# Optimization experiments

Hardware: AMD Instinct MI355X
Metric: run time of the kernel (lower is better)

The kernel has to match this reference:

```python
import jax, jax.numpy as jnp
import numpy as np

N_NODES = 100000
N_EDGES = 1600000
IN_CH = 128
HID = 128
OUT_CH = 64
N_GRAPHS = 512


def gcn_conv(x, edge_index, W, b):
    # GCNConv (PyG defaults): add self-loops, symmetric normalization
    # out = D^{-1/2} (A + I) D^{-1/2} X W + b
    n = x.shape[0]
    loop = jnp.arange(n, dtype=edge_index.dtype)
    src = jnp.concatenate([edge_index[0], loop])
    dst = jnp.concatenate([edge_index[1], loop])
    deg = jax.ops.segment_sum(jnp.ones_like(dst, x.dtype), dst, num_segments=n)
    dinv = jnp.where(deg > 0, jax.lax.rsqrt(deg), jnp.zeros_like(deg))
    norm = dinv[src] * dinv[dst]            # [E+N]
    h = x @ W                                # [N, out] transform first (dense GEMM)
    msg = h[src] * norm[:, None]             # gather + scale  [E+N, out]
    return jax.ops.segment_sum(msg, dst, num_segments=n) + b


def global_mean_pool(x, batch, num_graphs):
    sums = jax.ops.segment_sum(x, batch, num_segments=num_graphs)
    cnts = jax.ops.segment_sum(jnp.ones_like(batch, x.dtype), batch, num_segments=num_graphs)
    return sums / jnp.maximum(cnts, 1.0)[:, None]


def setup_inputs() -> dict:
    key = jax.random.key(0)
    ks = jax.random.split(key, 12)
    x = jax.random.normal(ks[0], (N_NODES, IN_CH), dtype=jnp.float32)
    edge_index = jax.random.randint(ks[1], (2, N_EDGES), 0, N_NODES, dtype=jnp.int64)
    batch = jnp.sort(jax.random.randint(ks[2], (N_NODES,), 0, N_GRAPHS, dtype=jnp.int64))
    def glorot(k, fi, fo):
        s = float(np.sqrt(6.0 / (fi + fo)))
        return jax.random.uniform(k, (fi, fo), jnp.float32, -s, s)
    W1 = glorot(ks[3], IN_CH, HID); b1 = jnp.zeros((HID,), jnp.float32)
    W2 = glorot(ks[4], HID, HID);   b2 = jnp.zeros((HID,), jnp.float32)
    W3 = glorot(ks[5], HID, HID);   b3 = jnp.zeros((HID,), jnp.float32)
    W4 = glorot(ks[6], HID, OUT_CH); b4 = jnp.zeros((OUT_CH,), jnp.float32)
    return {"x": x, "edge_index": edge_index, "batch": batch,
            "W1": W1, "b1": b1, "W2": W2, "b2": b2,
            "W3": W3, "b3": b3, "W4": W4, "b4": b4}


def reference(x, edge_index, batch, W1, b1, W2, b2, W3, b3, W4, b4):
    h = jax.nn.relu(gcn_conv(x, edge_index, W1, b1))
    h = jax.nn.relu(gcn_conv(h, edge_index, W2, b2))
    g = global_mean_pool(h, batch, N_GRAPHS)           # [G, HID]
    # MLP head; Dropout(0.2) is identity in eval mode
    g = jax.nn.relu(g @ W3 + b3)
    return g @ W4 + b4                                  # [G, OUT_CH]
```

## Files before the change

### kernel.cpp

```cpp
#include <hip/hip_runtime.h>

#define NN 100000
#define EE 1600000
#define CH 128
#define NG 512
#define OC 64

#define CSH 10
#define NCB 98
#define PBLK 256
#define PCHUNK 6250
#define SCAP 128

#define O_DINV   0
#define O_ROWS   100032
#define O_CNT    200064
#define O_PART   225152
#define O_OFFS   225280
#define O_START  225408
#define O_CSR    225984
#define O_HS     2726016
#define O_STG    9126080
#define O_WT1    9126080
#define O_WT2    9142464
#define O_A1     14800448

typedef __attribute__((ext_vector_type(8))) short short8v;
typedef __attribute__((ext_vector_type(4))) float float4v;

static __device__ __forceinline__ unsigned short f2bf(float x) {
  unsigned u = __float_as_uint(x);
  return (unsigned short)((u + 0x7FFFu + ((u >> 16) & 1u)) >> 16);
}
static __device__ __forceinline__ float bf2f(unsigned short h) {
  return __uint_as_float((unsigned)h << 16);
}
static __device__ __forceinline__ unsigned pack2(float a, float b) {
  return (unsigned)f2bf(a) | ((unsigned)f2bf(b) << 16);
}
static __device__ __forceinline__ float bflo(unsigned v) {
  return __uint_as_float(v << 16);
}
static __device__ __forceinline__ float bfhi(unsigned v) {
  return __uint_as_float(v & 0xFFFF0000u);
}

__global__ __launch_bounds__(1024) void k_part(const int* __restrict__ src,
                                               const int* __restrict__ dst,
                                               int* __restrict__ cnt,
                                               unsigned* __restrict__ stg) {
  __shared__ int hist[NCB];
  __shared__ int lcur[NCB];
  __shared__ unsigned lout[PCHUNK];
  int t = threadIdx.x;
  int e0 = blockIdx.x * PCHUNK;
  if (t < NCB) { hist[t] = 0; lcur[t] = 0; }
  __syncthreads();
  for (int e = e0 + t; e < e0 + PCHUNK; e += 1024)
    atomicAdd(&hist[dst[e] >> CSH], 1);
  __syncthreads();
  if (t == 0) {
    int s = 0;
    for (int i = 0; i < NCB; ++i) { int v = hist[i]; hist[i] = s; s += v; }
  }
  __syncthreads();
  for (int e = e0 + t; e < e0 + PCHUNK; e += 1024) {
    int d = dst[e];
    int b = d >> CSH;
    int p = hist[b] + atomicAdd(&lcur[b], 1);
    lout[p] = (unsigned)src[e] | ((unsigned)(d & 1023) << 17);
  }
  __syncthreads();
  int w = t >> 6, lane = t & 63;
  unsigned* mystg = stg + (size_t)blockIdx.x * NCB * SCAP;
  for (int b = w; b < NCB; b += 16) {
    int beg = hist[b];
    int end = (b == NCB - 1) ? PCHUNK : hist[b + 1];
    int n = min(end - beg, SCAP);
    for (int i = lane; i < n; i += 64) mystg[b * SCAP + i] = lout[beg + i];
    if (lane == 0) cnt[blockIdx.x * NCB + b] = n;
  }
}

__global__ __launch_bounds__(1024) void k_count(const unsigned* __restrict__ stg,
                                                const int* __restrict__ cnt,
                                                int* __restrict__ rows,
                                                int* __restrict__ part,
                                                float* __restrict__ dinv) {
  __shared__ int ldeg[1024];
  __shared__ int s[1024];
  int b = blockIdx.x;
  int t = threadIdx.x;
  int w = t >> 6, lane = t & 63;
  int gid = (b << CSH) + t;
  ldeg[t] = 0;
  __syncthreads();
  for (int blk = w; blk < PBLK; blk += 16) {
    int c = cnt[blk * NCB + b];
    const unsigned* p = stg + ((size_t)blk * NCB + b) * SCAP;
    for (int e = lane; e < c; e += 64) atomicAdd(&ldeg[p[e] >> 17], 1);
  }
  __syncthreads();
  int v = ldeg[t];
  if (gid < NN) dinv[gid] = rsqrtf((float)(v + 1));
  int pdeg = (v + 7) & ~7;
  s[t] = pdeg;
  __syncthreads();
  for (int off = 1; off < 1024; off <<= 1) {
    int u = (t >= off) ? s[t - off] : 0;
    __syncthreads();
    if (t >= off) s[t] += u;
    __syncthreads();
  }
  if (gid < NN) rows[gid] = s[t] - pdeg;
  if (t == 1023) part[b] = s[t];
}

__global__ void k_scan_part(const int* __restrict__ part, int* __restrict__ offs) {
  __shared__ int s[128];
  int t = threadIdx.x;
  int v = (t < NCB) ? part[t] : 0;
  s[t] = v;
  __syncthreads();
  for (int off = 1; off < 128; off <<= 1) {
    int u = (t >= off) ? s[t - off] : 0;
    __syncthreads();
    if (t >= off) s[t] += u;
    __syncthreads();
  }
  if (t < NCB) offs[t] = s[t] - v;
}

__global__ void k_scan_add(int* __restrict__ rows, const int* __restrict__ offs,
                           const int* __restrict__ part,
                           const int* __restrict__ batch, int* __restrict__ start) {
  int i = blockIdx.x * 256 + threadIdx.x;
  if (i >= NN) return;
  rows[i] += offs[i >> 10];
  if (i == 0) rows[NN] = offs[NCB - 1] + part[NCB - 1];
  int b = batch[i];
  int prev = (i == 0) ? -1 : batch[i - 1];
  for (int g = prev + 1; g <= b; ++g) start[g] = i;
  if (i == NN - 1)
    for (int g = b + 1; g <= NG; ++g) start[g] = NN;
}

__global__ __launch_bounds__(1024) void k_place(const unsigned* __restrict__ stg,
                                                const int* __restrict__ cnt,
                                                const int* __restrict__ rows,
                                                int* __restrict__ csr) {
  __shared__ int lrow[1024];
  __shared__ int lcur[1024];
  int b = blockIdx.x;
  int t = threadIdx.x;
  int w = t >> 6, lane = t & 63;
  int gid = (b << CSH) + t;
  lrow[t] = (gid < NN) ? rows[gid] : 0;
  lcur[t] = 0;
  __syncthreads();
  for (int blk = w; blk < PBLK; blk += 16) {
    int c = cnt[blk * NCB + b];
    const unsigned* p = stg + ((size_t)blk * NCB + b) * SCAP;
    for (int e = lane; e < c; e += 64) {
      unsigned x = p[e];
      int ld = x >> 17;
      int q = atomicAdd(&lcur[ld], 1);
      csr[lrow[ld] + q] = (int)(x & 0x1FFFFu);
    }
  }
  __syncthreads();
  int d = lcur[t];
  int pd = (d + 7) & ~7;
  int base = lrow[t];
  for (int i = d; i < pd; ++i) csr[base + i] = NN;
}

__global__ void k_wsplit(const float* __restrict__ W1, const float* __restrict__ W2,
                         unsigned short* __restrict__ wt1,
                         unsigned short* __restrict__ wt2) {
  int id = blockIdx.x * 256 + threadIdx.x;
  const float* W = (id < 16384) ? W1 : W2;
  unsigned short* wt = (id < 16384) ? wt1 : wt2;
  int i = id & 16383;
  int k = i >> 7, n = i & 127;
  float w = W[i];
  unsigned short h = f2bf(w);
  unsigned short l = f2bf(w - bf2f(h));
  wt[n * 128 + k] = h;
  wt[16384 + n * 128 + k] = l;
}

__global__ __launch_bounds__(256) void k_gemm_mfma(
    const float* __restrict__ X, const unsigned short* __restrict__ wth,
    const unsigned short* __restrict__ wtl, const float* __restrict__ dinv,
    unsigned short* __restrict__ Hs) {
  __shared__ __align__(16) unsigned short sWh[64 * 136];
  __shared__ __align__(16) unsigned short sWl[64 * 136];
  __shared__ __align__(16) unsigned short sXh[128 * 40];
  __shared__ __align__(16) unsigned short sXl[128 * 40];

  const int t = threadIdx.x;
  const int w = t >> 6, lane = t & 63;
  const int quad = lane >> 4, lr = lane & 15;
  const int row0 = blockIdx.x * 128;
  const int col0 = blockIdx.y * 64;

  if (blockIdx.x == 0 && blockIdx.y == 0 && t < 64)
    *(unsigned*)&Hs[(size_t)NN * CH + t * 2] = 0u;

#pragma unroll
  for (int j = 0; j < 8; ++j) {
    int id = t + j * 256;
    int n = id >> 5, kk = (id & 31) * 4;
    *(ushort4*)&sWh[n * 136 + kk] = *(const ushort4*)&wth[(col0 + n) * 128 + kk];
    *(ushort4*)&sWl[n * 136 + kk] = *(const ushort4*)&wtl[(col0 + n) * 128 + kk];
  }

  float4v acc[2][4];
#pragma unroll
  for (int mi = 0; mi < 2; ++mi)
#pragma unroll
    for (int ni = 0; ni < 4; ++ni) acc[mi][ni] = (float4v){0.f, 0.f, 0.f, 0.f};

  for (int ks = 0; ks < 4; ++ks) {
    const int k0 = ks * 32;
    if (ks) __syncthreads();
#pragma unroll
    for (int i = 0; i < 4; ++i) {
      int row = i * 32 + (t >> 3);
      int seg = t & 7;
      int gr = row0 + row;
      float4 xv = {0.f, 0.f, 0.f, 0.f};
      if (gr < NN) xv = *(const float4*)&X[(size_t)gr * CH + k0 + seg * 4];
      ushort4 h, l;
      h.x = f2bf(xv.x); l.x = f2bf(xv.x - bf2f(h.x));
      h.y = f2bf(xv.y); l.y = f2bf(xv.y - bf2f(h.y));
      h.z = f2bf(xv.z); l.z = f2bf(xv.z - bf2f(h.z));
      h.w = f2bf(xv.w); l.w = f2bf(xv.w - bf2f(h.w));
      *(ushort4*)&sXh[row * 40 + seg * 4] = h;
      *(ushort4*)&sXl[row * 40 + seg * 4] = l;
    }
    __syncthreads();

    short8v ah[2], al[2];
#pragma unroll
    for (int mi = 0; mi < 2; ++mi) {
      int r = w * 32 + mi * 16 + lr;
      ah[mi] = *(const short8v*)&sXh[r * 40 + quad * 8];
      al[mi] = *(const short8v*)&sXl[r * 40 + quad * 8];
    }
#pragma unroll
    for (int ni = 0; ni < 4; ++ni) {
      int n = ni * 16 + lr;
      short8v bh = *(const short8v*)&sWh[n * 136 + k0 + quad * 8];
      short8v bl = *(const short8v*)&sWl[n * 136 + k0 + quad * 8];
#pragma unroll
      for (int mi = 0; mi < 2; ++mi) {
        acc[mi][ni] = __builtin_amdgcn_mfma_f32_16x16x32_bf16(ah[mi], bh, acc[mi][ni], 0, 0, 0);
        acc[mi][ni] = __builtin_amdgcn_mfma_f32_16x16x32_bf16(ah[mi], bl, acc[mi][ni], 0, 0, 0);
        acc[mi][ni] = __builtin_amdgcn_mfma_f32_16x16x32_bf16(al[mi], bh, acc[mi][ni], 0, 0, 0);
      }
    }
  }

#pragma unroll
  for (int mi = 0; mi < 2; ++mi) {
#pragma unroll
    for (int r = 0; r < 4; ++r) {
      int grow = row0 + w * 32 + mi * 16 + quad * 4 + r;
      if (grow < NN) {
        float d = dinv[grow];
#pragma unroll
        for (int ni = 0; ni < 4; ++ni)
          Hs[(size_t)grow * CH + col0 + ni * 16 + lr] = f2bf(d * acc[mi][ni][r]);
      }
    }
  }
}

__global__ __launch_bounds__(256) void k_gemm_bf(
    const unsigned short* __restrict__ A, const unsigned short* __restrict__ wth,
    const unsigned short* __restrict__ wtl, const float* __restrict__ dinv,
    unsigned short* __restrict__ Hs) {
  __shared__ __align__(16) unsigned short sWh[64 * 136];
  __shared__ __align__(16) unsigned short sWl[64 * 136];
  __shared__ __align__(16) unsigned short sA[128 * 40];

  const int t = threadIdx.x;
  const int w = t >> 6, lane = t & 63;
  const int quad = lane >> 4, lr = lane & 15;
  const int row0 = blockIdx.x * 128;
  const int col0 = blockIdx.y * 64;

  if (blockIdx.x == 0 && blockIdx.y == 0 && t < 64)
    *(unsigned*)&Hs[(size_t)NN * CH + t * 2] = 0u;

#pragma unroll
  for (int j = 0; j < 8; ++j) {
    int id = t + j * 256;
    int n = id >> 5, kk = (id & 31) * 4;
    *(ushort4*)&sWh[n * 136 + kk] = *(const ushort4*)&wth[(col0 + n) * 128 + kk];
    *(ushort4*)&sWl[n * 136 + kk] = *(const ushort4*)&wtl[(col0 + n) * 128 + kk];
  }

  float4v acc[2][4];
#pragma unroll
  for (int mi = 0; mi < 2; ++mi)
#pragma unroll
    for (int ni = 0; ni < 4; ++ni) acc[mi][ni] = (float4v){0.f, 0.f, 0.f, 0.f};

  for (int ks = 0; ks < 4; ++ks) {
    const int k0 = ks * 32;
    if (ks) __syncthreads();
#pragma unroll
    for (int i = 0; i < 2; ++i) {
      int id = t + i * 256;
      int row = id >> 2, seg = id & 3;
      int gr = row0 + row;
      ushort4 v = {0, 0, 0, 0};
      if (gr < NN) v = *(const ushort4*)&A[(size_t)gr * CH + k0 + seg * 8];
      *(ushort4*)&sA[row * 40 + seg * 8] = v;
      ushort4 v2 = {0, 0, 0, 0};
      if (gr < NN) v2 = *(const ushort4*)&A[(size_t)gr * CH + k0 + seg * 8 + 4];
      *(ushort4*)&sA[row * 40 + seg * 8 + 4] = v2;
    }
    __syncthreads();

    short8v ah[2];
#pragma unroll
    for (int mi = 0; mi < 2; ++mi) {
      int r = w * 32 + mi * 16 + lr;
      ah[mi] = *(const short8v*)&sA[r * 40 + quad * 8];
    }
#pragma unroll
    for (int ni = 0; ni < 4; ++ni) {
      int n = ni * 16 + lr;
      short8v bh = *(const short8v*)&sWh[n * 136 + k0 + quad * 8];
      short8v bl = *(const short8v*)&sWl[n * 136 + k0 + quad * 8];
#pragma unroll
      for (int mi = 0; mi < 2; ++mi) {
        acc[mi][ni] = __builtin_amdgcn_mfma_f32_16x16x32_bf16(ah[mi], bh, acc[mi][ni], 0, 0, 0);
        acc[mi][ni] = __builtin_amdgcn_mfma_f32_16x16x32_bf16(ah[mi], bl, acc[mi][ni], 0, 0, 0);
      }
    }
  }

#pragma unroll
  for (int mi = 0; mi < 2; ++mi) {
#pragma unroll
    for (int r = 0; r < 4; ++r) {
      int grow = row0 + w * 32 + mi * 16 + quad * 4 + r;
      if (grow < NN) {
        float d = dinv[grow];
#pragma unroll
        for (int ni = 0; ni < 4; ++ni)
          Hs[(size_t)grow * CH + col0 + ni * 16 + lr] = f2bf(d * acc[mi][ni][r]);
      }
    }
  }
}

__global__ __launch_bounds__(256) void k_aggregate(
    const uint2* __restrict__ H2, const int* __restrict__ rows,
    const int* __restrict__ csr, const float* __restrict__ dinv,
    const float* __restrict__ bias, uint2* __restrict__ out) {
  int node = blockIdx.x * 4 + (threadIdx.x >> 6);
  if (node >= NN) return;
  int lane = threadIdx.x & 63;
  int h = lane >> 5, li = lane & 31;
  float a0 = 0.f, a1 = 0.f, a2 = 0.f, a3 = 0.f;
  int e0 = rows[node], e1 = rows[node + 1];
  int nr = (e1 - e0) >> 3;
  if (nr) {
    const int* cp = csr + e0 + h;
    uint2 va[4], vb[4];

#define LOADQ(buf)                                                          \
  do {                                                                      \
    unsigned s0_ = (unsigned)cp[0], s1_ = (unsigned)cp[2];                  \
    unsigned s2_ = (unsigned)cp[4], s3_ = (unsigned)cp[6];                  \
    buf[0] = H2[(s0_ << 5) | li];                                           \
    buf[1] = H2[(s1_ << 5) | li];                                           \
    buf[2] = H2[(s2_ << 5) | li];                                           \
    buf[3] = H2[(s3_ << 5) | li];                                           \
    cp += 8;                                                                \
  } while (0)

#define ACCQ(buf)                                                           \
  do {                                                                      \
    _Pragma("unroll")                                                       \
    for (int k_ = 0; k_ < 4; ++k_) {                                        \
      a0 += bflo(buf[k_].x); a1 += bfhi(buf[k_].x);                         \
      a2 += bflo(buf[k_].y); a3 += bfhi(buf[k_].y);                         \
    }                                                                       \
  } while (0)

    LOADQ(va);
    int rem = nr - 1;
    while (rem >= 2) {
      LOADQ(vb); ACCQ(va);
      LOADQ(va); ACCQ(vb);
      rem -= 2;
    }
    if (rem) { LOADQ(vb); ACCQ(va); ACCQ(vb); }
    else     { ACCQ(va); }
#undef LOADQ
#undef ACCQ
  }
  a0 += __shfl_xor(a0, 32);
  a1 += __shfl_xor(a1, 32);
  a2 += __shfl_xor(a2, 32);
  a3 += __shfl_xor(a3, 32);
  uint2 sv = H2[((unsigned)node << 5) | li];
  a0 += bflo(sv.x); a1 += bfhi(sv.x);
  a2 += bflo(sv.y); a3 += bfhi(sv.y);
  float d = dinv[node];
  float4 b4 = *(const float4*)&bias[li << 2];
  float o0 = fmaxf(fmaf(d, a0, b4.x), 0.f);
  float o1 = fmaxf(fmaf(d, a1, b4.y), 0.f);
  float o2 = fmaxf(fmaf(d, a2, b4.z), 0.f);
  float o3 = fmaxf(fmaf(d, a3, b4.w), 0.f);
  if (!h)
    out[((unsigned)node << 5) | li] = make_uint2(pack2(o0, o1), pack2(o2, o3));
}

__global__ __launch_bounds__(256) void k_head(
    const unsigned short* __restrict__ A, const int* __restrict__ start,
    const float* __restrict__ W3, const float* __restrict__ b3,
    const float* __restrict__ W4, const float* __restrict__ b4,
    float* __restrict__ out) {
  __shared__ float pooled[128];
  __shared__ float part[128];
  __shared__ float g1[128];
  int g = blockIdx.x;
  int c = threadIdx.x & 127;
  int half = threadIdx.x >> 7;
  int s0 = start[g], s1 = start[g + 1];
  float sum = 0.f;
  for (int i = s0 + half; i < s1; i += 2)
    sum += bf2f(A[(size_t)i * CH + c]);
  if (half) part[c] = sum;
  __syncthreads();
  if (!half) {
    float n = fmaxf((float)(s1 - s0), 1.0f);
    pooled[c] = (sum + part[c]) / n;
  }
  __syncthreads();
  if (threadIdx.x < 128) {
    float acc = b3[c];
    for (int k = 0; k < 128; ++k) acc += pooled[k] * W3[k * CH + c];
    g1[c] = fmaxf(acc, 0.f);
  }
  __syncthreads();
  if (threadIdx.x < 64) {
    float acc = b4[threadIdx.x];
    for (int k = 0; k < 128; ++k) acc += g1[k] * W4[k * OC + threadIdx.x];
    out[(size_t)g * OC + threadIdx.x] = acc;
  }
}

extern "C" void kernel_launch(void* const* d_in, const int* in_sizes, int n_in,
                              void* d_out, int out_size, void* d_ws, size_t ws_size,
                              hipStream_t stream) {
  const float* X   = (const float*)d_in[0];
  const int* ei    = (const int*)d_in[1];
  const int* batch = (const int*)d_in[2];
  const float* W1  = (const float*)d_in[3];
  const float* b1  = (const float*)d_in[4];
  const float* W2  = (const float*)d_in[5];
  const float* b2  = (const float*)d_in[6];
  const float* W3  = (const float*)d_in[7];
  const float* b3  = (const float*)d_in[8];
  const float* W4  = (const float*)d_in[9];
  const float* b4  = (const float*)d_in[10];
  float* out = (float*)d_out;
  float* ws = (float*)d_ws;

  const int* src = ei;
  const int* dst = ei + EE;

  float* dinv = ws + O_DINV;
  int* rows   = (int*)(ws + O_ROWS);
  int* cnt    = (int*)(ws + O_CNT);
  int* part   = (int*)(ws + O_PART);
  int* offs   = (int*)(ws + O_OFFS);
  int* start  = (int*)(ws + O_START);
  int* csr    = (int*)(ws + O_CSR);
  unsigned short* Hs = (unsigned short*)(ws + O_HS);
  unsigned* stg = (unsigned*)(ws + O_STG);
  unsigned short* wt1 = (unsigned short*)(ws + O_WT1);
  unsigned short* wt2 = (unsigned short*)(ws + O_WT2);
  unsigned short* A1 = (unsigned short*)(ws + O_A1);

  k_part<<<PBLK, 1024, 0, stream>>>(src, dst, cnt, stg);
  k_count<<<NCB, 1024, 0, stream>>>(stg, cnt, rows, part, dinv);
  k_scan_part<<<1, 128, 0, stream>>>(part, offs);
  k_scan_add<<<(NN + 255) / 256, 256, 0, stream>>>(rows, offs, part, batch, start);
  k_place<<<NCB, 1024, 0, stream>>>(stg, cnt, rows, csr);
  k_wsplit<<<128, 256, 0, stream>>>(W1, W2, wt1, wt2);

  dim3 ggrid((NN + 127) / 128, 2);
  k_gemm_mfma<<<ggrid, 256, 0, stream>>>(X, wt1, wt1 + 16384, dinv, Hs);
  k_aggregate<<<(NN + 3) / 4, 256, 0, stream>>>((const uint2*)Hs, rows, csr, dinv, b1, (uint2*)A1);
  k_gemm_bf<<<ggrid, 256, 0, stream>>>(A1, wt2, wt2 + 16384, dinv, Hs);
  k_aggregate<<<(NN + 3) / 4, 256, 0, stream>>>((const uint2*)Hs, rows, csr, dinv, b2, (uint2*)A1);

  k_head<<<NG, 256, 0, stream>>>(A1, start, W3, b3, W4, b4, out);
}
```

Before: 376.8 us.

## Compute full 128-column GEMM tiles per block with weights read from global memory; vectorize pooling

The two GEMM kernels now compute all 128 output columns per block instead of splitting columns across two blocks. This halves the grid and removes the redundant X load and bf16 split per column half. Weight fragments are read directly from global memory (through cache) instead of being staged in shared memory, which drops the weight LDS fill but doubles the accumulator registers and may lower occupancy. The head kernel's mean pooling now uses 16 row-groups with 8-wide vector loads and a shared-memory reduction, in place of two scalar-load halves.

```diff
diff --git a/kernel.cpp b/kernel.cpp
--- a/kernel.cpp
+++ b/kernel.cpp
@@ -194,8 +194,6 @@
     const float* __restrict__ X, const unsigned short* __restrict__ wth,
     const unsigned short* __restrict__ wtl, const float* __restrict__ dinv,
     unsigned short* __restrict__ Hs) {
-  __shared__ __align__(16) unsigned short sWh[64 * 136];
-  __shared__ __align__(16) unsigned short sWl[64 * 136];
   __shared__ __align__(16) unsigned short sXh[128 * 40];
   __shared__ __align__(16) unsigned short sXl[128 * 40];
 
@@ -203,24 +201,15 @@
   const int w = t >> 6, lane = t & 63;
   const int quad = lane >> 4, lr = lane & 15;
   const int row0 = blockIdx.x * 128;
-  const int col0 = blockIdx.y * 64;
-
-  if (blockIdx.x == 0 && blockIdx.y == 0 && t < 64)
+
+  if (blockIdx.x == 0 && t < 64)
     *(unsigned*)&Hs[(size_t)NN * CH + t * 2] = 0u;
 
-#pragma unroll
-  for (int j = 0; j < 8; ++j) {
-    int id = t + j * 256;
-    int n = id >> 5, kk = (id & 31) * 4;
-    *(ushort4*)&sWh[n * 136 + kk] = *(const ushort4*)&wth[(col0 + n) * 128 + kk];
-    *(ushort4*)&sWl[n * 136 + kk] = *(const ushort4*)&wtl[(col0 + n) * 128 + kk];
-  }
-
-  float4v acc[2][4];
+  float4v acc[2][8];
 #pragma unroll
   for (int mi = 0; mi < 2; ++mi)
 #pragma unroll
-    for (int ni = 0; ni < 4; ++ni) acc[mi][ni] = (float4v){0.f, 0.f, 0.f, 0.f};
+    for (int ni = 0; ni < 8; ++ni) acc[mi][ni] = (float4v){0.f, 0.f, 0.f, 0.f};
 
   for (int ks = 0; ks < 4; ++ks) {
     const int k0 = ks * 32;
@@ -250,10 +239,10 @@
       al[mi] = *(const short8v*)&sXl[r * 40 + quad * 8];
     }
 #pragma unroll
-    for (int ni = 0; ni < 4; ++ni) {
+    for (int ni = 0; ni < 8; ++ni) {
       int n = ni * 16 + lr;
-      short8v bh = *(const short8v*)&sWh[n * 136 + k0 + quad * 8];
-      short8v bl = *(const short8v*)&sWl[n * 136 + k0 + quad * 8];
+      short8v bh = *(const short8v*)&wth[n * 128 + k0 + quad * 8];
+      short8v bl = *(const short8v*)&wtl[n * 128 + k0 + quad * 8];
 #pragma unroll
       for (int mi = 0; mi < 2; ++mi) {
         acc[mi][ni] = __builtin_amdgcn_mfma_f32_16x16x32_bf16(ah[mi], bh, acc[mi][ni], 0, 0, 0);
@@ -271,8 +260,8 @@
       if (grow < NN) {
         float d = dinv[grow];
 #pragma unroll
-        for (int ni = 0; ni < 4; ++ni)
-          Hs[(size_t)grow * CH + col0 + ni * 16 + lr] = f2bf(d * acc[mi][ni][r]);
+        for (int ni = 0; ni < 8; ++ni)
+          Hs[(size_t)grow * CH + ni * 16 + lr] = f2bf(d * acc[mi][ni][r]);
       }
     }
   }
@@ -282,32 +271,21 @@
     const unsigned short* __restrict__ A, const unsigned short* __restrict__ wth,
     const unsigned short* __restrict__ wtl, const float* __restrict__ dinv,
     unsigned short* __restrict__ Hs) {
-  __shared__ __align__(16) unsigned short sWh[64 * 136];
-  __shared__ __align__(16) unsigned short sWl[64 * 136];
   __shared__ __align__(16) unsigned short sA[128 * 40];
 
   const int t = threadIdx.x;
   const int w = t >> 6, lane = t & 63;
   const int quad = lane >> 4, lr = lane & 15;
   const int row0 = blockIdx.x * 128;
-  const int col0 = blockIdx.y * 64;
-
-  if (blockIdx.x == 0 && blockIdx.y == 0 && t < 64)
+
+  if (blockIdx.x == 0 && t < 64)
     *(unsigned*)&Hs[(size_t)NN * CH + t * 2] = 0u;
 
-#pragma unroll
-  for (int j = 0; j < 8; ++j) {
-    int id = t + j * 256;
-    int n = id >> 5, kk = (id & 31) * 4;
-    *(ushort4*)&sWh[n * 136 + kk] = *(const ushort4*)&wth[(col0 + n) * 128 + kk];
-    *(ushort4*)&sWl[n * 136 + kk] = *(const ushort4*)&wtl[(col0 + n) * 128 + kk];
-  }
-
-  float4v acc[2][4];
+  float4v acc[2][8];
 #pragma unroll
   for (int mi = 0; mi < 2; ++mi)
 #pragma unroll
-    for (int ni = 0; ni < 4; ++ni) acc[mi][ni] = (float4v){0.f, 0.f, 0.f, 0.f};
+    for (int ni = 0; ni < 8; ++ni) acc[mi][ni] = (float4v){0.f, 0.f, 0.f, 0.f};
 
   for (int ks = 0; ks < 4; ++ks) {
     const int k0 = ks * 32;
@@ -333,10 +311,10 @@
       ah[mi] = *(const short8v*)&sA[r * 40 + quad * 8];
     }
 #pragma unroll
-    for (int ni = 0; ni < 4; ++ni) {
+    for (int ni = 0; ni < 8; ++ni) {
       int n = ni * 16 + lr;
-      short8v bh = *(const short8v*)&sWh[n * 136 + k0 + quad * 8];
-      short8v bl = *(const short8v*)&sWl[n * 136 + k0 + quad * 8];
+      short8v bh = *(const short8v*)&wth[n * 128 + k0 + quad * 8];
+      short8v bl = *(const short8v*)&wtl[n * 128 + k0 + quad * 8];
 #pragma unroll
       for (int mi = 0; mi < 2; ++mi) {
         acc[mi][ni] = __builtin_amdgcn_mfma_f32_16x16x32_bf16(ah[mi], bh, acc[mi][ni], 0, 0, 0);
@@ -353,8 +331,8 @@
       if (grow < NN) {
         float d = dinv[grow];
 #pragma unroll
-        for (int ni = 0; ni < 4; ++ni)
-          Hs[(size_t)grow * CH + col0 + ni * 16 + lr] = f2bf(d * acc[mi][ni][r]);
+        for (int ni = 0; ni < 8; ++ni)
+          Hs[(size_t)grow * CH + ni * 16 + lr] = f2bf(d * acc[mi][ni][r]);
       }
     }
   }
@@ -429,33 +407,41 @@
     const float* __restrict__ W3, const float* __restrict__ b3,
     const float* __restrict__ W4, const float* __restrict__ b4,
     float* __restrict__ out) {
+  __shared__ float ppart[16][128];
   __shared__ float pooled[128];
-  __shared__ float part[128];
   __shared__ float g1[128];
   int g = blockIdx.x;
-  int c = threadIdx.x & 127;
-  int half = threadIdx.x >> 7;
+  int t = threadIdx.x;
+  int c8 = t & 15;
+  int r = t >> 4;
   int s0 = start[g], s1 = start[g + 1];
-  float sum = 0.f;
-  for (int i = s0 + half; i < s1; i += 2)
-    sum += bf2f(A[(size_t)i * CH + c]);
-  if (half) part[c] = sum;
-  __syncthreads();
-  if (!half) {
+  float s[8] = {0.f, 0.f, 0.f, 0.f, 0.f, 0.f, 0.f, 0.f};
+  for (int i = s0 + r; i < s1; i += 16) {
+    short8v v = *(const short8v*)&A[(size_t)i * CH + c8 * 8];
+#pragma unroll
+    for (int j = 0; j < 8; ++j) s[j] += bf2f((unsigned short)v[j]);
+  }
+#pragma unroll
+  for (int j = 0; j < 8; ++j) ppart[r][c8 * 8 + j] = s[j];
+  __syncthreads();
+  if (t < 128) {
     float n = fmaxf((float)(s1 - s0), 1.0f);
-    pooled[c] = (sum + part[c]) / n;
-  }
-  __syncthreads();
-  if (threadIdx.x < 128) {
-    float acc = b3[c];
-    for (int k = 0; k < 128; ++k) acc += pooled[k] * W3[k * CH + c];
-    g1[c] = fmaxf(acc, 0.f);
-  }
-  __syncthreads();
-  if (threadIdx.x < 64) {
-    float acc = b4[threadIdx.x];
-    for (int k = 0; k < 128; ++k) acc += g1[k] * W4[k * OC + threadIdx.x];
-    out[(size_t)g * OC + threadIdx.x] = acc;
+    float acc = 0.f;
+#pragma unroll
+    for (int rr = 0; rr < 16; ++rr) acc += ppart[rr][t];
+    pooled[t] = acc / n;
+  }
+  __syncthreads();
+  if (t < 128) {
+    float acc = b3[t];
+    for (int k = 0; k < 128; ++k) acc += pooled[k] * W3[k * CH + t];
+    g1[t] = fmaxf(acc, 0.f);
+  }
+  __syncthreads();
+  if (t < 64) {
+    float acc = b4[t];
+    for (int k = 0; k < 128; ++k) acc += g1[k] * W4[k * OC + t];
+    out[(size_t)g * OC + t] = acc;
   }
 }
 
@@ -499,7 +485,7 @@
   k_place<<<NCB, 1024, 0, stream>>>(stg, cnt, rows, csr);
   k_wsplit<<<128, 256, 0, stream>>>(W1, W2, wt1, wt2);
 
-  dim3 ggrid((NN + 127) / 128, 2);
+  int ggrid = (NN + 127) / 128;
   k_gemm_mfma<<<ggrid, 256, 0, stream>>>(X, wt1, wt1 + 16384, dinv, Hs);
   k_aggregate<<<(NN + 3) / 4, 256, 0, stream>>>((const uint2*)Hs, rows, csr, dinv, b1, (uint2*)A1);
   k_gemm_bf<<<ggrid, 256, 0, stream>>>(A1, wt2, wt2 + 16384, dinv, Hs);
```

New measurement: 372.7 us. No clear change (-1.1%).
